# Kernel tuning notes

Hardware: AMD Instinct MI355X
Metric: run time of the kernel (lower is better)

Reference implementation:

```python
import jax, jax.numpy as jnp
import numpy as np

B, N, F, FE, FG = 4, 512, 128, 128, 128
OUT, MID, H = 128, 128, 8
HEAD = OUT // H      # 16
MH = MID // H        # 16
LN_EPS = 1e-5


def setup_inputs() -> dict:
    key = jax.random.key(0)
    ks = jax.random.split(key, 24)
    s = 0.02
    inp = {
        "node_fts": jax.random.normal(ks[0], (B, N, F), jnp.float32),
        "edge_fts": jax.random.normal(ks[1], (B, N, N, FE), jnp.float32),
        "graph_fts": jax.random.normal(ks[2], (B, FG), jnp.float32),
        "adj_mat": jax.random.randint(ks[3], (B, N, N), 0, 2).astype(jnp.float32),
        "hidden": jax.random.normal(ks[4], (B, N, OUT), jnp.float32),
        # hk.Linear params
        "m_w": jax.random.normal(ks[5], (F, OUT), jnp.float32) * s,
        "m_b": jnp.zeros((OUT,), jnp.float32),
        "skip_w": jax.random.normal(ks[6], (F, OUT), jnp.float32) * s,
        "skip_b": jnp.zeros((OUT,), jnp.float32),
        "w1_w": jax.random.normal(ks[7], (F, MID), jnp.float32) * s,
        "w1_b": jnp.zeros((MID,), jnp.float32),
        "w2_w": jax.random.normal(ks[8], (F, MID), jnp.float32) * s,
        "w2_b": jnp.zeros((MID,), jnp.float32),
        "we_w": jax.random.normal(ks[9], (FE, MID), jnp.float32) * s,
        "we_b": jnp.zeros((MID,), jnp.float32),
        "wg_w": jax.random.normal(ks[10], (FG, MID), jnp.float32) * s,
        "wg_b": jnp.zeros((MID,), jnp.float32),
        # per-head Linear(1): stacked weight (H, MH) and bias (H,)
        "a_w": jax.random.normal(ks[11], (H, MH), jnp.float32) * s,
        "a_b": jnp.zeros((H,), jnp.float32),
        # LayerNorm params
        "ln_scale": jnp.ones((OUT,), jnp.float32),
        "ln_offset": jnp.zeros((OUT,), jnp.float32),
    }
    return inp


def reference(node_fts, edge_fts, graph_fts, adj_mat, hidden,
              m_w, m_b, skip_w, skip_b,
              w1_w, w1_b, w2_w, w2_b, we_w, we_b, wg_w, wg_b,
              a_w, a_b, ln_scale, ln_offset):
    b, n, _ = node_fts.shape
    # values: (B, H, N, HEAD)
    values = (node_fts @ m_w + m_b).reshape(b, n, H, HEAD).transpose(0, 2, 1, 3)
    pre1 = node_fts @ w1_w + w1_b            # (B, N, MID) -> receiver i
    pre2 = node_fts @ w2_w + w2_b            # (B, N, MID) -> sender j
    pre_e = edge_fts @ we_w + we_b           # (B, N, N, MID)
    pre_g = graph_fts @ wg_w + wg_b          # (B, MID)
    # broadcast-sum: (B, N, N, MID); axis1 = i (expand pre1), axis2 = j (expand pre2)
    pre = pre1[:, None, :, :] + pre2[:, :, None, :] + pre_e + pre_g[:, None, None, :]
    pre = pre.reshape(b, n, n, H, MH)
    # per-head logit: leaky_relu then Linear(1) -> (B, H, N, N)
    logits = jnp.einsum("bijhm,hm->bhij", jax.nn.leaky_relu(pre), a_w)
    logits = logits + a_b[None, :, None, None]
    bias = (adj_mat - 1.0) * 1e9             # (B, N, N)
    coefs = jax.nn.softmax(logits + bias[:, None, :, :], axis=-1)
    ret = jnp.matmul(coefs, values)          # (B, H, N, HEAD)
    ret = ret.transpose(0, 2, 1, 3).reshape(b, n, OUT)
    ret = ret + (node_fts @ skip_w + skip_b)  # residual
    ret = jax.nn.relu(ret)                    # activation
    # LayerNorm over last axis (haiku defaults, eps=1e-5)
    mu = jnp.mean(ret, axis=-1, keepdims=True)
    var = jnp.var(ret, axis=-1, keepdims=True)
    ret = (ret - mu) * jax.lax.rsqrt(var + LN_EPS) * ln_scale + ln_offset
    return ret
```

## Files before the change

kernel.cpp:

```cpp
#include <hip/hip_runtime.h>
#include <hip/hip_bf16.h>

typedef __bf16 bf16x8 __attribute__((ext_vector_type(8)));
typedef float f32x4 __attribute__((ext_vector_type(4)));

#define B_ 4
#define N_ 512
#define D_ 128
#define H_ 8
#define LSTR 264

__device__ __forceinline__ unsigned short f2bf(float f) {
    unsigned int u = __float_as_uint(f);
    unsigned int r = (u + 0x7FFFu + ((u >> 16) & 1u)) >> 16;
    return (unsigned short)r;
}

__global__ __launch_bounds__(128) void prep_kernel(
    const float* __restrict__ node,
    const float* __restrict__ graph,
    const float* __restrict__ m_w, const float* __restrict__ m_b,
    const float* __restrict__ skip_w, const float* __restrict__ skip_b,
    const float* __restrict__ w1_b,
    const float* __restrict__ w2_w, const float* __restrict__ w2_b,
    const float* __restrict__ we_b,
    const float* __restrict__ wg_w, const float* __restrict__ wg_b,
    float* __restrict__ values_ws,
    float* __restrict__ combo_ws,
    float* __restrict__ skip_ws)
{
    __shared__ float s_node[4][D_];
    __shared__ float s_graph[D_];
    const int col = threadIdx.x;
    const int b  = blockIdx.x >> 7;
    const int n0 = (blockIdx.x & 127) * 4;

    for (int r = 0; r < 4; ++r)
        s_node[r][col] = node[(size_t)(b * N_ + n0 + r) * D_ + col];
    s_graph[col] = graph[b * D_ + col];
    __syncthreads();

    float gacc = 0.f;
#pragma unroll 8
    for (int k = 0; k < D_; ++k)
        gacc += s_graph[k] * wg_w[k * D_ + col];
    const float cbase = gacc + wg_b[col] + w1_b[col] + we_b[col] + w2_b[col];

    for (int r = 0; r < 4; ++r) {
        float v = 0.f, s = 0.f, c = 0.f;
#pragma unroll 8
        for (int k = 0; k < D_; ++k) {
            const float nf = s_node[r][k];
            v += nf * m_w[k * D_ + col];
            s += nf * skip_w[k * D_ + col];
            c += nf * w2_w[k * D_ + col];
        }
        const size_t row = (size_t)(b * N_ + n0 + r) * D_ + col;
        values_ws[row] = v + m_b[col];
        skip_ws[row]   = s + skip_b[col];
        combo_ws[row]  = c + cbase;
    }
}

__global__ __launch_bounds__(256, 3) void gat_kernel(
    const float* __restrict__ edge,
    const float* __restrict__ node,
    const float* __restrict__ adj,
    const float* __restrict__ we_w,
    const float* __restrict__ w1_w,
    const float* __restrict__ a_w,
    const float* __restrict__ a_b,
    const float* __restrict__ ln_scale,
    const float* __restrict__ ln_offset,
    const float* __restrict__ values_ws,
    const float* __restrict__ combo_ws,
    const float* __restrict__ skip_ws,
    float* __restrict__ out)
{
    __shared__ __align__(16) unsigned short sA[64 * LSTR];
    __shared__ float sLogit[H_ * N_];
    __shared__ float sBias[N_];
    __shared__ float sPart[2 * D_];
    __shared__ float sRed[4];

    const int tid  = threadIdx.x;
    const int wave = tid >> 6;
    const int lane = tid & 63;
    const int quad = lane >> 4;
    const int mm   = lane & 15;

    const int b = blockIdx.x >> 9;
    const int i = blockIdx.x & (N_ - 1);

    for (int j = tid; j < N_; j += 256)
        sBias[j] = (adj[(size_t)(b * N_ + i) * N_ + j] - 1.0f) * 1e9f;

    const int h0 = wave * 2;
    bf16x8 breg[2][8];
#pragma unroll
    for (int nti = 0; nti < 2; ++nti) {
        const int n = (h0 + nti) * 16 + mm;
#pragma unroll
        for (int kc = 0; kc < 8; ++kc) {
            union { unsigned short u[8]; bf16x8 v; } t;
#pragma unroll
            for (int e = 0; e < 8; ++e) {
                const int k = kc * 32 + quad * 8 + e;
                const float w = (k < 128) ? we_w[k * D_ + n] : w1_w[(k - 128) * D_ + n];
                t.u[e] = f2bf(w);
            }
            breg[nti][kc] = t.v;
        }
    }

    float creg[2], awreg[2], abreg[2];
#pragma unroll
    for (int nti = 0; nti < 2; ++nti) {
        creg[nti]  = combo_ws[(size_t)(b * N_ + i) * D_ + (h0 + nti) * 16 + mm];
        awreg[nti] = a_w[(h0 + nti) * 16 + mm];
        abreg[nti] = a_b[h0 + nti];
    }

    const size_t edge_base = (size_t)(b * N_ + i) * N_ * D_;
    const size_t node_base = (size_t)b * N_ * D_;

    for (int pass = 0; pass < 8; ++pass) {
        const int j0 = pass * 64;
        __syncthreads();
        for (int c = tid; c < 2048; c += 256) {
            const int row  = c >> 5;
            const int part = c & 31;
            const float* src = (part < 16)
                ? (edge + edge_base + (size_t)(j0 + row) * D_ + part * 8)
                : (node + node_base + (size_t)(j0 + row) * D_ + (part - 16) * 8);
            const float4 f0 = ((const float4*)src)[0];
            const float4 f1 = ((const float4*)src)[1];
            uint4 w;
            w.x = (unsigned)f2bf(f0.x) | ((unsigned)f2bf(f0.y) << 16);
            w.y = (unsigned)f2bf(f0.z) | ((unsigned)f2bf(f0.w) << 16);
            w.z = (unsigned)f2bf(f1.x) | ((unsigned)f2bf(f1.y) << 16);
            w.w = (unsigned)f2bf(f1.z) | ((unsigned)f2bf(f1.w) << 16);
            ((uint4*)sA)[row * 33 + part] = w;
        }
        __syncthreads();

        f32x4 acc[4][2];
#pragma unroll
        for (int mt = 0; mt < 4; ++mt)
#pragma unroll
            for (int nti = 0; nti < 2; ++nti) {
                f32x4 z = {0.f, 0.f, 0.f, 0.f};
                acc[mt][nti] = z;
            }

#pragma unroll
        for (int kc = 0; kc < 8; ++kc) {
            bf16x8 a[4];
#pragma unroll
            for (int mt = 0; mt < 4; ++mt)
                a[mt] = *(const bf16x8*)(sA + (mt * 16 + mm) * LSTR + kc * 32 + quad * 8);
#pragma unroll
            for (int mt = 0; mt < 4; ++mt)
#pragma unroll
                for (int nti = 0; nti < 2; ++nti)
                    acc[mt][nti] = __builtin_amdgcn_mfma_f32_16x16x32_bf16(
                        a[mt], breg[nti][kc], acc[mt][nti], 0, 0, 0);
        }

#pragma unroll
        for (int mt = 0; mt < 4; ++mt)
#pragma unroll
            for (int nti = 0; nti < 2; ++nti)
#pragma unroll
                for (int r = 0; r < 4; ++r) {
                    float v = acc[mt][nti][r] + creg[nti];
                    v = v > 0.f ? v : 0.01f * v;
                    float p = v * awreg[nti];
                    p += __shfl_xor(p, 1);
                    p += __shfl_xor(p, 2);
                    p += __shfl_xor(p, 4);
                    p += __shfl_xor(p, 8);
                    if (mm == 0) {
                        const int j = j0 + mt * 16 + quad * 4 + r;
                        sLogit[(h0 + nti) * N_ + j] = p + abreg[nti] + sBias[j];
                    }
                }
    }
    __syncthreads();

#pragma unroll
    for (int hi = 0; hi < 2; ++hi) {
        float* lrow = sLogit + (h0 + hi) * N_;
        float v[8];
        float mx = -3.0e38f;
#pragma unroll
        for (int t = 0; t < 8; ++t) { v[t] = lrow[lane + t * 64]; mx = fmaxf(mx, v[t]); }
#pragma unroll
        for (int s = 1; s < 64; s <<= 1) mx = fmaxf(mx, __shfl_xor(mx, s));
        float sum = 0.f;
#pragma unroll
        for (int t = 0; t < 8; ++t) { v[t] = __expf(v[t] - mx); sum += v[t]; }
#pragma unroll
        for (int s = 1; s < 64; s <<= 1) sum += __shfl_xor(sum, s);
        const float inv = 1.0f / sum;
#pragma unroll
        for (int t = 0; t < 8; ++t) lrow[lane + t * 64] = v[t] * inv;
    }
    __syncthreads();

    const int m = tid & 127;
    const int half = tid >> 7;
    const float* crow = sLogit + (m >> 4) * N_;
    const float* vp = values_ws + (size_t)b * N_ * D_ + m;
    float av = 0.f;
    for (int j = half; j < N_; j += 2)
        av += crow[j] * vp[(size_t)j * D_];
    sPart[half * D_ + m] = av;
    __syncthreads();

    float r = 0.f;
    if (tid < 128) {
        r = sPart[m] + sPart[D_ + m] + skip_ws[(size_t)(b * N_ + i) * D_ + m];
        r = fmaxf(r, 0.f);
        float s1 = r, s2 = r * r;
#pragma unroll
        for (int s = 1; s < 64; s <<= 1) { s1 += __shfl_xor(s1, s); s2 += __shfl_xor(s2, s); }
        if (lane == 0) { sRed[wave * 2] = s1; sRed[wave * 2 + 1] = s2; }
    }
    __syncthreads();
    if (tid < 128) {
        const float s1 = sRed[0] + sRed[2];
        const float s2 = sRed[1] + sRed[3];
        const float mu  = s1 * (1.0f / 128.0f);
        const float var = s2 * (1.0f / 128.0f) - mu * mu;
        const float o = (r - mu) * rsqrtf(var + 1e-5f) * ln_scale[m] + ln_offset[m];
        out[(size_t)(b * N_ + i) * D_ + m] = o;
    }
}

extern "C" void kernel_launch(void* const* d_in, const int* in_sizes, int n_in,
                              void* d_out, int out_size, void* d_ws, size_t ws_size,
                              hipStream_t stream) {
    const float* node   = (const float*)d_in[0];
    const float* edge   = (const float*)d_in[1];
    const float* graph  = (const float*)d_in[2];
    const float* adj    = (const float*)d_in[3];
    const float* m_w    = (const float*)d_in[5];
    const float* m_b    = (const float*)d_in[6];
    const float* skip_w = (const float*)d_in[7];
    const float* skip_b = (const float*)d_in[8];
    const float* w1_w   = (const float*)d_in[9];
    const float* w1_b   = (const float*)d_in[10];
    const float* w2_w   = (const float*)d_in[11];
    const float* w2_b   = (const float*)d_in[12];
    const float* we_w   = (const float*)d_in[13];
    const float* we_b   = (const float*)d_in[14];
    const float* wg_w   = (const float*)d_in[15];
    const float* wg_b   = (const float*)d_in[16];
    const float* a_w    = (const float*)d_in[17];
    const float* a_b    = (const float*)d_in[18];
    const float* ln_s   = (const float*)d_in[19];
    const float* ln_o   = (const float*)d_in[20];

    char* ws = (char*)d_ws;
    float* values_ws = (float*)ws;
    float* combo_ws  = (float*)(ws + (1u << 20));
    float* skip_ws   = (float*)(ws + (2u << 20));

    hipLaunchKernelGGL(prep_kernel, dim3(512), dim3(128), 0, stream,
        node, graph, m_w, m_b, skip_w, skip_b, w1_b, w2_w, w2_b, we_b, wg_w, wg_b,
        values_ws, combo_ws, skip_ws);

    hipLaunchKernelGGL(gat_kernel, dim3(B_ * N_), dim3(256), 0, stream,
        edge, node, adj, we_w, w1_w, a_w, a_b, ln_s, ln_o,
        values_ws, combo_ws, skip_ws, (float*)d_out);
}
```

Baseline: 1.109 ms.

## Prefetch edge tiles into registers, pre-convert node features to bf16, swap MFMA operands

```diff
diff --git a/kernel.cpp b/kernel.cpp
--- a/kernel.cpp
+++ b/kernel.cpp
@@ -27,7 +27,8 @@
     const float* __restrict__ wg_w, const float* __restrict__ wg_b,
     float* __restrict__ values_ws,
     float* __restrict__ combo_ws,
-    float* __restrict__ skip_ws)
+    float* __restrict__ skip_ws,
+    unsigned short* __restrict__ nodebf)
 {
     __shared__ float s_node[4][D_];
     __shared__ float s_graph[D_];
@@ -59,12 +60,12 @@
         values_ws[row] = v + m_b[col];
         skip_ws[row]   = s + skip_b[col];
         combo_ws[row]  = c + cbase;
+        nodebf[row]    = f2bf(s_node[r][col]);
     }
 }
 
 __global__ __launch_bounds__(256, 3) void gat_kernel(
     const float* __restrict__ edge,
-    const float* __restrict__ node,
     const float* __restrict__ adj,
     const float* __restrict__ we_w,
     const float* __restrict__ w1_w,
@@ -75,6 +76,7 @@
     const float* __restrict__ values_ws,
     const float* __restrict__ combo_ws,
     const float* __restrict__ skip_ws,
+    const unsigned short* __restrict__ nodebf,
     float* __restrict__ out)
 {
     __shared__ __align__(16) unsigned short sA[64 * LSTR];
@@ -113,36 +115,64 @@
         }
     }
 
-    float creg[2], awreg[2], abreg[2];
+    float creg[2][4], awreg[2][4], abreg[2];
 #pragma unroll
     for (int nti = 0; nti < 2; ++nti) {
-        creg[nti]  = combo_ws[(size_t)(b * N_ + i) * D_ + (h0 + nti) * 16 + mm];
-        awreg[nti] = a_w[(h0 + nti) * 16 + mm];
         abreg[nti] = a_b[h0 + nti];
+#pragma unroll
+        for (int r = 0; r < 4; ++r) {
+            creg[nti][r]  = combo_ws[(size_t)(b * N_ + i) * D_ + (h0 + nti) * 16 + quad * 4 + r];
+            awreg[nti][r] = a_w[(h0 + nti) * 16 + quad * 4 + r];
+        }
     }
 
     const size_t edge_base = (size_t)(b * N_ + i) * N_ * D_;
-    const size_t node_base = (size_t)b * N_ * D_;
+    const size_t nb_base   = (size_t)b * N_ * D_;
+
+    const int srow = tid >> 4;
+    const int ch   = tid & 15;
+
+    float4 ef[4][2];
+
+#define LOAD_EDGE(J0)                                                              \
+    {                                                                              \
+        _Pragma("unroll")                                                          \
+        for (int k = 0; k < 4; ++k) {                                              \
+            const float* ep = edge + edge_base +                                   \
+                (size_t)((J0) + srow + 16 * k) * D_ + ch * 8;                      \
+            ef[k][0] = ((const float4*)ep)[0];                                     \
+            ef[k][1] = ((const float4*)ep)[1];                                     \
+        }                                                                          \
+    }
+
+    LOAD_EDGE(0);
 
     for (int pass = 0; pass < 8; ++pass) {
         const int j0 = pass * 64;
         __syncthreads();
-        for (int c = tid; c < 2048; c += 256) {
-            const int row  = c >> 5;
-            const int part = c & 31;
-            const float* src = (part < 16)
-                ? (edge + edge_base + (size_t)(j0 + row) * D_ + part * 8)
-                : (node + node_base + (size_t)(j0 + row) * D_ + (part - 16) * 8);
-            const float4 f0 = ((const float4*)src)[0];
-            const float4 f1 = ((const float4*)src)[1];
+
+        uint4 nf[4];
+#pragma unroll
+        for (int k = 0; k < 4; ++k)
+            nf[k] = *(const uint4*)(nodebf + nb_base +
+                                    (size_t)(j0 + srow + 16 * k) * D_ + ch * 8);
+#pragma unroll
+        for (int k = 0; k < 4; ++k) {
+            const int row = srow + 16 * k;
             uint4 w;
-            w.x = (unsigned)f2bf(f0.x) | ((unsigned)f2bf(f0.y) << 16);
-            w.y = (unsigned)f2bf(f0.z) | ((unsigned)f2bf(f0.w) << 16);
-            w.z = (unsigned)f2bf(f1.x) | ((unsigned)f2bf(f1.y) << 16);
-            w.w = (unsigned)f2bf(f1.z) | ((unsigned)f2bf(f1.w) << 16);
-            ((uint4*)sA)[row * 33 + part] = w;
-        }
+            w.x = (unsigned)f2bf(ef[k][0].x) | ((unsigned)f2bf(ef[k][0].y) << 16);
+            w.y = (unsigned)f2bf(ef[k][0].z) | ((unsigned)f2bf(ef[k][0].w) << 16);
+            w.z = (unsigned)f2bf(ef[k][1].x) | ((unsigned)f2bf(ef[k][1].y) << 16);
+            w.w = (unsigned)f2bf(ef[k][1].z) | ((unsigned)f2bf(ef[k][1].w) << 16);
+            ((uint4*)sA)[row * 33 + ch] = w;
+        }
+#pragma unroll
+        for (int k = 0; k < 4; ++k)
+            ((uint4*)sA)[(srow + 16 * k) * 33 + 16 + ch] = nf[k];
+
         __syncthreads();
+
+        if (pass < 7) LOAD_EDGE(j0 + 64);
 
         f32x4 acc[4][2];
 #pragma unroll
@@ -164,28 +194,29 @@
 #pragma unroll
                 for (int nti = 0; nti < 2; ++nti)
                     acc[mt][nti] = __builtin_amdgcn_mfma_f32_16x16x32_bf16(
-                        a[mt], breg[nti][kc], acc[mt][nti], 0, 0, 0);
-        }
-
-#pragma unroll
-        for (int mt = 0; mt < 4; ++mt)
-#pragma unroll
-            for (int nti = 0; nti < 2; ++nti)
+                        breg[nti][kc], a[mt], acc[mt][nti], 0, 0, 0);
+        }
+
+#pragma unroll
+        for (int mt = 0; mt < 4; ++mt) {
+            const int j = j0 + mt * 16 + mm;
+#pragma unroll
+            for (int nti = 0; nti < 2; ++nti) {
+                float p = 0.f;
 #pragma unroll
                 for (int r = 0; r < 4; ++r) {
-                    float v = acc[mt][nti][r] + creg[nti];
+                    float v = acc[mt][nti][r] + creg[nti][r];
                     v = v > 0.f ? v : 0.01f * v;
-                    float p = v * awreg[nti];
-                    p += __shfl_xor(p, 1);
-                    p += __shfl_xor(p, 2);
-                    p += __shfl_xor(p, 4);
-                    p += __shfl_xor(p, 8);
-                    if (mm == 0) {
-                        const int j = j0 + mt * 16 + quad * 4 + r;
-                        sLogit[(h0 + nti) * N_ + j] = p + abreg[nti] + sBias[j];
-                    }
+                    p += v * awreg[nti][r];
                 }
-    }
+                p += __shfl_xor(p, 16);
+                p += __shfl_xor(p, 32);
+                if (quad == 0)
+                    sLogit[(h0 + nti) * N_ + j] = p + abreg[nti] + sBias[j];
+            }
+        }
+    }
+#undef LOAD_EDGE
     __syncthreads();
 
 #pragma unroll
@@ -266,12 +297,13 @@
     float* values_ws = (float*)ws;
     float* combo_ws  = (float*)(ws + (1u << 20));
     float* skip_ws   = (float*)(ws + (2u << 20));
+    unsigned short* nodebf = (unsigned short*)(ws + (3u << 20));
 
     hipLaunchKernelGGL(prep_kernel, dim3(512), dim3(128), 0, stream,
         node, graph, m_w, m_b, skip_w, skip_b, w1_b, w2_w, w2_b, we_b, wg_w, wg_b,
-        values_ws, combo_ws, skip_ws);
+        values_ws, combo_ws, skip_ws, nodebf);
 
     hipLaunchKernelGGL(gat_kernel, dim3(B_ * N_), dim3(256), 0, stream,
-        edge, node, adj, we_w, w1_w, a_w, a_b, ln_s, ln_o,
-        values_ws, combo_ws, skip_ws, (float*)d_out);
+        edge, adj, we_w, w1_w, a_w, a_b, ln_s, ln_o,
+        values_ws, combo_ws, skip_ws, nodebf, (float*)d_out);
 }
```

New measurement: 1.028 ms. 1.08x faster.
